# Performance work log

Measured on AMD Instinct MI355X. Metric: run time of the kernel, lower is better.

## Reference

```python
import jax, jax.numpy as jnp
import numpy as np

N = 50000
E = 800000
C = 128          # in = hidden = out channels
R = 16           # num_relations
NB = 4           # num_bases
EPS = 1e-5


def setup_inputs() -> dict:
    key = jax.random.key(0)
    ks = jax.random.split(key, 20)
    node_features = jax.random.normal(ks[0], (N, C), dtype=jnp.float32)
    src = jax.random.randint(ks[1], (E,), 0, N, dtype=jnp.int32)
    rel = jax.random.randint(ks[2], (E,), 0, R, dtype=jnp.int32)
    dst = jax.random.randint(ks[3], (E,), 0, N, dtype=jnp.int32)
    edge_triples = jnp.stack([src, rel, dst], axis=1)  # [E,3]
    s = 0.05
    inp = {
        "node_features": node_features,
        "edge_triples": edge_triples,
        "num_nodes": N,
        "input_w": jax.random.normal(ks[4], (C, C), jnp.float32) * s,
        "input_b": jnp.zeros((C,), jnp.float32),
    }
    for i in range(2):
        k = jax.random.split(ks[5 + i], 4)
        inp[f"basis{i}"] = jax.random.normal(k[0], (NB, C, C), jnp.float32) * s
        inp[f"att{i}"] = jax.random.normal(k[1], (R, NB), jnp.float32) * s
        inp[f"root_w{i}"] = jax.random.normal(k[2], (C, C), jnp.float32) * s
        inp[f"root_b{i}"] = jnp.zeros((C,), jnp.float32)
        inp[f"ln_g{i}"] = jnp.ones((C,), jnp.float32)
        inp[f"ln_b{i}"] = jnp.zeros((C,), jnp.float32)
    return inp


def _layer_norm(x, g, b):
    mu = jnp.mean(x, axis=-1, keepdims=True)
    var = jnp.mean(jnp.square(x - mu), axis=-1, keepdims=True)
    return (x - mu) * jax.lax.rsqrt(var + EPS) * g + b


def _rel_conv(x, edge_triples, num_nodes, basis, att, root_w, root_b):
    # x: [N,C]; basis: [NB,C,O]; att: [R,NB]
    src = edge_triples[:, 0]
    rel = edge_triples[:, 1]
    dst = edge_triples[:, 2]
    # weights = einsum('rb,bio->rio'); messages_e = x[src] @ weights[rel]
    # = sum_b att[rel,b] * (x @ basis[b])[src]  (same math, no [E,C,O] tensor)
    xb = jnp.einsum('ni,bio->bno', x, basis)      # [NB,N,O]
    coef = att[rel]                                # [E,NB]
    out_dim = basis.shape[-1]
    msg = jnp.zeros((src.shape[0], out_dim), x.dtype)
    for b in range(basis.shape[0]):                # small fixed loop over bases
        msg = msg + coef[:, b, None] * xb[b][src]
    deg = jax.ops.segment_sum(jnp.ones_like(dst, dtype=x.dtype), dst,
                              num_segments=num_nodes)
    deg_inv = jnp.where(deg > 0, 1.0 / deg, 0.0)
    msg = msg * deg_inv[dst][:, None]
    out = jax.ops.segment_sum(msg, dst, num_segments=num_nodes)
    return out + x @ root_w + root_b


def reference(node_features, edge_triples, num_nodes, input_w, input_b,
              basis0, att0, root_w0, root_b0, ln_g0, ln_b0,
              basis1, att1, root_w1, root_b1, ln_g1, ln_b1):
    x = node_features @ input_w + input_b
    x = _rel_conv(x, edge_triples, num_nodes, basis0, att0, root_w0, root_b0)
    x = _layer_norm(x, ln_g0, ln_b0)
    x = jax.nn.relu(x)  # dropout is identity in eval mode
    x = _rel_conv(x, edge_triples, num_nodes, basis1, att1, root_w1, root_b1)
    x = _layer_norm(x, ln_g1, ln_b1)
    return x
```

## Files before the change

kernel.cpp:

```cpp
#include <hip/hip_runtime.h>
#include <hip/hip_bf16.h>

#define NN 50000
#define EE 800000

typedef __bf16 bf16x8 __attribute__((ext_vector_type(8)));
typedef float f32x4 __attribute__((ext_vector_type(4)));

__device__ inline float bf2f(unsigned int u) {
    union { unsigned int i; float f; } x; x.i = (u & 0xFFFFu) << 16; return x.f;
}
__device__ inline float bf2fh(unsigned int u) {
    union { unsigned int i; float f; } x; x.i = u & 0xFFFF0000u; return x.f;
}
__device__ inline void bf8_to_f(bf16x8 v, float* f) {
    const unsigned int* u = (const unsigned int*)&v;
    f[0] = bf2f(u[0]); f[1] = bf2fh(u[0]);
    f[2] = bf2f(u[1]); f[3] = bf2fh(u[1]);
    f[4] = bf2f(u[2]); f[5] = bf2fh(u[2]);
    f[6] = bf2f(u[3]); f[7] = bf2fh(u[3]);
}

__global__ void k_zero(int* __restrict__ deg, int* __restrict__ curs) {
    int i = blockIdx.x * 256 + threadIdx.x;
    if (i < NN) { deg[i] = 0; curs[i] = 0; }
}

__global__ void k_deg(const int* __restrict__ et, int* __restrict__ deg) {
    int e = blockIdx.x * 256 + threadIdx.x;
    if (e < EE) atomicAdd(&deg[et[e * 3 + 2]], 1);
}

__global__ void k_scan1(const int* __restrict__ deg, int* __restrict__ incl, int* __restrict__ bsum) {
    __shared__ int s[1024];
    int i = blockIdx.x * 1024 + threadIdx.x;
    int v = (i < NN) ? deg[i] : 0;
    s[threadIdx.x] = v;
    __syncthreads();
    for (int off = 1; off < 1024; off <<= 1) {
        int t = (threadIdx.x >= off) ? s[threadIdx.x - off] : 0;
        __syncthreads();
        s[threadIdx.x] += t;
        __syncthreads();
    }
    if (i < NN) incl[i] = s[threadIdx.x];
    if (threadIdx.x == 1023) bsum[blockIdx.x] = s[1023];
}

__global__ void k_scan2(const int* __restrict__ bsum, int* __restrict__ boff) {
    if (threadIdx.x == 0 && blockIdx.x == 0) {
        int acc = 0;
        for (int i = 0; i < 49; ++i) { boff[i] = acc; acc += bsum[i]; }
    }
}

__global__ void k_scan3(const int* __restrict__ incl, const int* __restrict__ deg,
                        const int* __restrict__ boff, int* __restrict__ row_start) {
    int i = blockIdx.x * 1024 + threadIdx.x;
    if (i < NN) row_start[i] = incl[i] - deg[i] + boff[blockIdx.x];
}

__global__ void k_fill(const int* __restrict__ et, const int* __restrict__ row_start,
                       int* __restrict__ cursor, int* __restrict__ perm) {
    int e = blockIdx.x * 256 + threadIdx.x;
    if (e >= EE) return;
    int src = et[e * 3 + 0];
    int rel = et[e * 3 + 1];
    int dst = et[e * 3 + 2];
    int pos = row_start[dst] + atomicAdd(&cursor[dst], 1);
    perm[pos] = src | (rel << 16);
}

__global__ void k_prep(const float* __restrict__ iw,
                       const float* __restrict__ basis0, const float* __restrict__ rootw0,
                       const float* __restrict__ basis1, const float* __restrict__ rootw1,
                       __bf16* __restrict__ WtInF, __bf16* __restrict__ WtF0, __bf16* __restrict__ WtF1) {
    int t = blockIdx.x * 256 + threadIdx.x;
    if (t < 2048) {
        int lane = t & 63, grp = t >> 6;
        int kk = grp & 3, nblk = grp >> 2;
        int col = nblk * 16 + (lane & 15);
        int k0 = kk * 32 + (lane >> 4) * 8;
        bf16x8 v;
        #pragma unroll
        for (int j = 0; j < 8; ++j) v[j] = (__bf16)iw[(size_t)(k0 + j) * 128 + col];
        *(bf16x8*)(WtInF + (size_t)t * 8) = v;
        return;
    }
    t -= 2048;
    const float* basis = basis0; const float* rootw = rootw0; __bf16* W = WtF0;
    if (t >= 10240) { t -= 10240; basis = basis1; rootw = rootw1; W = WtF1; }
    if (t >= 10240) return;
    int lane = t & 63, grp = t >> 6;
    int kk = grp % 20, nblk = grp / 20;
    int col = nblk * 16 + (lane & 15);
    int k0 = kk * 32 + (lane >> 4) * 8;
    bf16x8 v;
    #pragma unroll
    for (int j = 0; j < 8; ++j) {
        int k = k0 + j;
        float f = (k < 512) ? basis[(size_t)(k >> 7) * 16384 + (size_t)(k & 127) * 128 + col]
                            : rootw[(size_t)(k - 512) * 128 + col];
        v[j] = (__bf16)f;
    }
    *(bf16x8*)(W + (size_t)t * 8) = v;
}

__global__ void k_gemm_in(const float* __restrict__ A, const __bf16* __restrict__ WtInF,
                          const float* __restrict__ bias, __bf16* __restrict__ out, int M) {
    const int tid = threadIdx.x, wave = tid >> 6, lane = tid & 63;
    const int wr = wave >> 1, wc = wave & 1;
    const int l15 = lane & 15, lhi = lane >> 4;
    f32x4 acc[2][4] = {};
    #define LDAI(dst, KK) do { \
        _Pragma("unroll") \
        for (int m = 0; m < 2; ++m) { \
            int rw = blockIdx.x * 64 + wr * 32 + m * 16 + l15; \
            rw = rw < M ? rw : M - 1; \
            const float* ap = A + (size_t)rw * 128 + (KK) * 32 + lhi * 8; \
            float4 v0 = *(const float4*)ap, v1 = *(const float4*)(ap + 4); \
            bf16x8 f; \
            f[0]=(__bf16)v0.x; f[1]=(__bf16)v0.y; f[2]=(__bf16)v0.z; f[3]=(__bf16)v0.w; \
            f[4]=(__bf16)v1.x; f[5]=(__bf16)v1.y; f[6]=(__bf16)v1.z; f[7]=(__bf16)v1.w; \
            dst[m] = f; \
        } } while (0)
    #define LDBI(dst, KK) do { \
        _Pragma("unroll") \
        for (int n = 0; n < 4; ++n) \
            dst[n] = *(const bf16x8*)(WtInF + (((size_t)(wc * 4 + n) * 4 + (KK)) * 64 + lane) * 8); \
        } while (0)
    #define MMI(AA, BB) do { \
        _Pragma("unroll") for (int m = 0; m < 2; ++m) \
        _Pragma("unroll") for (int n = 0; n < 4; ++n) \
            acc[m][n] = __builtin_amdgcn_mfma_f32_16x16x32_bf16(AA[m], BB[n], acc[m][n], 0, 0, 0); \
        } while (0)
    bf16x8 aP[2], bP[4], aQ[2], bQ[4];
    LDAI(aP, 0); LDBI(bP, 0);
    #pragma unroll
    for (int tstep = 0; tstep < 2; ++tstep) {
        LDAI(aQ, 2 * tstep + 1); LDBI(bQ, 2 * tstep + 1);
        MMI(aP, bP);
        if (tstep < 1) { LDAI(aP, 2 * tstep + 2); LDBI(bP, 2 * tstep + 2); }
        MMI(aQ, bQ);
    }
    #pragma unroll
    for (int m = 0; m < 2; ++m)
        #pragma unroll
        for (int j = 0; j < 4; ++j) {
            int row = blockIdx.x * 64 + wr * 32 + m * 16 + lhi * 4 + j;
            if (row >= M) continue;
            #pragma unroll
            for (int n = 0; n < 4; ++n) {
                int col = wc * 64 + n * 16 + l15;
                out[(size_t)row * 128 + col] = (__bf16)(acc[m][n][j] + bias[col]);
            }
        }
}

__global__ void k_agg4(const __bf16* __restrict__ x, const int* __restrict__ perm,
                       const int* __restrict__ rowst, const int* __restrict__ deg,
                       const float* __restrict__ att, __bf16* __restrict__ aggF,
                       int nodeOff, int nodeCnt) {
    __shared__ float4 satt[16];
    if (threadIdx.x < 16) satt[threadIdx.x] = ((const float4*)att)[threadIdx.x];
    __syncthreads();
    int local = blockIdx.x * 4 + (threadIdx.x >> 6);
    if (local >= nodeCnt) return;
    int lane = threadIdx.x & 63;
    int e4 = lane >> 4, c8 = lane & 15;
    int node = nodeOff + local;
    int start = rowst[node], cnt = deg[node];
    float acc[4][8] = {};
    int nIt = (cnt + 3) >> 2;
    for (int it = 0; it < nIt; it += 2) {
        int eA = it * 4 + e4, eB = eA + 4;
        bool vA = eA < cnt, vB = eB < cnt;
        int pA = vA ? perm[start + eA] : 0;
        int pB = vB ? perm[start + eB] : 0;
        bf16x8 uA = *(const bf16x8*)(x + (size_t)(pA & 0xFFFF) * 128 + c8 * 8);
        bf16x8 uB = *(const bf16x8*)(x + (size_t)(pB & 0xFFFF) * 128 + c8 * 8);
        float4 cA = satt[pA >> 16];
        float4 cB = satt[pB >> 16];
        if (!vA) cA = make_float4(0.f, 0.f, 0.f, 0.f);
        if (!vB) cB = make_float4(0.f, 0.f, 0.f, 0.f);
        float fA[8], fB[8];
        bf8_to_f(uA, fA);
        bf8_to_f(uB, fB);
        #pragma unroll
        for (int j = 0; j < 8; ++j) {
            acc[0][j] += cA.x * fA[j]; acc[1][j] += cA.y * fA[j];
            acc[2][j] += cA.z * fA[j]; acc[3][j] += cA.w * fA[j];
        }
        #pragma unroll
        for (int j = 0; j < 8; ++j) {
            acc[0][j] += cB.x * fB[j]; acc[1][j] += cB.y * fB[j];
            acc[2][j] += cB.z * fB[j]; acc[3][j] += cB.w * fB[j];
        }
    }
    float dinv = (cnt > 0) ? 1.f / (float)cnt : 0.f;
    #pragma unroll
    for (int b = 0; b < 4; ++b)
        #pragma unroll
        for (int j = 0; j < 8; ++j) {
            float v = acc[b][j];
            v += __shfl_xor(v, 16);
            v += __shfl_xor(v, 32);
            acc[b][j] = v * dinv;
        }
    bf16x8 o;
    #pragma unroll
    for (int j = 0; j < 8; ++j) {
        float v = (e4 == 0) ? acc[0][j] : (e4 == 1) ? acc[1][j] : (e4 == 2) ? acc[2][j] : acc[3][j];
        o[j] = (__bf16)v;
    }
    size_t idx8 = (((size_t)(local >> 4) * 16 + e4 * 4 + (c8 >> 2)) * 64 + (c8 & 3) * 16 + (local & 15)) * 8;
    *(bf16x8*)(aggF + idx8) = o;
}

template<int OUTF>
__global__ void k_gemm_layer(const __bf16* __restrict__ aggF, const __bf16* __restrict__ x,
                             const __bf16* __restrict__ WtF, const float* __restrict__ rb,
                             const float* __restrict__ g, const float* __restrict__ bb,
                             __bf16* __restrict__ outB, float* __restrict__ outF,
                             int rowOff, int nodeCnt) {
    __shared__ float red[2][2][64];
    __shared__ float murs[2][64];
    const int tid = threadIdx.x, wave = tid >> 6, lane = tid & 63;
    const int wr = wave >> 1, wc = wave & 1;
    const int l15 = lane & 15, lhi = lane >> 4;
    const int rowgrpBase = blockIdx.x * 4 + wr * 2;
    f32x4 acc[2][4] = {};
    #define LDA(dst, KK) do { \
        _Pragma("unroll") \
        for (int m = 0; m < 2; ++m) { \
            if ((KK) < 16) { \
                dst[m] = *(const bf16x8*)(aggF + (((size_t)(rowgrpBase + m) * 16 + (KK)) * 64 + lane) * 8); \
            } else { \
                int rw = blockIdx.x * 64 + wr * 32 + m * 16 + l15; \
                rw = rw < nodeCnt ? rw : nodeCnt - 1; \
                dst[m] = *(const bf16x8*)(x + (size_t)(rowOff + rw) * 128 + ((KK) - 16) * 32 + lhi * 8); \
            } \
        } } while (0)
    #define LDB(dst, KK) do { \
        _Pragma("unroll") \
        for (int n = 0; n < 4; ++n) \
            dst[n] = *(const bf16x8*)(WtF + (((size_t)(wc * 4 + n) * 20 + (KK)) * 64 + lane) * 8); \
        } while (0)
    #define MM(AA, BB) do { \
        _Pragma("unroll") for (int m = 0; m < 2; ++m) \
        _Pragma("unroll") for (int n = 0; n < 4; ++n) \
            acc[m][n] = __builtin_amdgcn_mfma_f32_16x16x32_bf16(AA[m], BB[n], acc[m][n], 0, 0, 0); \
        } while (0)
    bf16x8 aP[2], bP[4], aQ[2], bQ[4];
    LDA(aP, 0); LDB(bP, 0);
    #pragma unroll
    for (int t = 0; t < 10; ++t) {
        LDA(aQ, 2 * t + 1); LDB(bQ, 2 * t + 1);
        MM(aP, bP);
        if (t < 9) { LDA(aP, 2 * t + 2); LDB(bP, 2 * t + 2); }
        MM(aQ, bQ);
    }
    float colb[4];
    #pragma unroll
    for (int n = 0; n < 4; ++n) colb[n] = rb[wc * 64 + n * 16 + l15];
    #pragma unroll
    for (int m = 0; m < 2; ++m)
        #pragma unroll
        for (int j = 0; j < 4; ++j) {
            float s = 0.f, q = 0.f;
            #pragma unroll
            for (int n = 0; n < 4; ++n) {
                float v = acc[m][n][j] + colb[n];
                acc[m][n][j] = v;
                s += v; q += v * v;
            }
            #pragma unroll
            for (int o = 1; o < 16; o <<= 1) { s += __shfl_xor(s, o); q += __shfl_xor(q, o); }
            if (l15 == 0) {
                int r = wr * 32 + m * 16 + lhi * 4 + j;
                red[0][wc][r] = s; red[1][wc][r] = q;
            }
        }
    __syncthreads();
    if (tid < 64) {
        float s = red[0][0][tid] + red[0][1][tid];
        float q = red[1][0][tid] + red[1][1][tid];
        float mu = s * (1.f / 128.f);
        float var = q * (1.f / 128.f) - mu * mu;
        murs[0][tid] = mu;
        murs[1][tid] = rsqrtf(var + 1e-5f);
    }
    __syncthreads();
    float gg[4], gb[4];
    #pragma unroll
    for (int n = 0; n < 4; ++n) {
        int col = wc * 64 + n * 16 + l15;
        gg[n] = g[col]; gb[n] = bb[col];
    }
    #pragma unroll
    for (int m = 0; m < 2; ++m)
        #pragma unroll
        for (int j = 0; j < 4; ++j) {
            int rblk = wr * 32 + m * 16 + lhi * 4 + j;
            int lr = blockIdx.x * 64 + rblk;
            if (lr >= nodeCnt) continue;
            float mu = murs[0][rblk], rs = murs[1][rblk];
            size_t rowbase = (size_t)(rowOff + lr) * 128;
            #pragma unroll
            for (int n = 0; n < 4; ++n) {
                int col = wc * 64 + n * 16 + l15;
                float v = (acc[m][n][j] - mu) * rs * gg[n] + gb[n];
                if (OUTF == 0) { v = fmaxf(v, 0.f); outB[rowbase + col] = (__bf16)v; }
                else           { outF[rowbase + col] = v; }
            }
        }
}

extern "C" void kernel_launch(void* const* d_in, const int* in_sizes, int n_in,
                              void* d_out, int out_size, void* d_ws, size_t ws_size,
                              hipStream_t stream) {
    const float* nf      = (const float*)d_in[0];
    const int*   et      = (const int*)d_in[1];
    const float* input_w = (const float*)d_in[3];
    const float* input_b = (const float*)d_in[4];
    const float* basis0  = (const float*)d_in[5];
    const float* att0    = (const float*)d_in[6];
    const float* rootw0  = (const float*)d_in[7];
    const float* rootb0  = (const float*)d_in[8];
    const float* lng0    = (const float*)d_in[9];
    const float* lnb0    = (const float*)d_in[10];
    const float* basis1  = (const float*)d_in[11];
    const float* att1    = (const float*)d_in[12];
    const float* rootw1  = (const float*)d_in[13];
    const float* rootb1  = (const float*)d_in[14];
    const float* lng1    = (const float*)d_in[15];
    const float* lnb1    = (const float*)d_in[16];
    (void)in_sizes; (void)n_in; (void)out_size;

    char* ws = (char*)d_ws;
    size_t off = 0;
    auto carve = [&](size_t bytes) { char* p = ws + off; off = (off + bytes + 255) & ~(size_t)255; return p; };
    __bf16* x0    = (__bf16*)carve((size_t)NN * 128 * 2);
    __bf16* x1    = (__bf16*)carve((size_t)NN * 128 * 2);
    __bf16* WtInF = (__bf16*)carve((size_t)128 * 128 * 2);
    __bf16* WtF0  = (__bf16*)carve((size_t)128 * 640 * 2);
    __bf16* WtF1  = (__bf16*)carve((size_t)128 * 640 * 2);
    int*    deg   = (int*)carve((size_t)NN * 4);
    int*    incl  = (int*)carve((size_t)NN * 4);
    int*    rowst = (int*)carve((size_t)NN * 4);
    int*    curs  = (int*)carve((size_t)NN * 4);
    int*    bsum  = (int*)carve(64 * 4);
    int*    boff  = (int*)carve(64 * 4);
    int*    perm  = (int*)carve((size_t)EE * 4 + 64);
    size_t remain = (ws_size > off + 4096) ? (ws_size - off - 4096) : 0;
    long long maxNodes = (long long)(remain / 1024);
    int chunkN = (maxNodes >= NN) ? NN : (int)maxNodes;
    if (chunkN < 512) chunkN = 512;
    chunkN = (chunkN + 63) & ~63;
    __bf16* aggF = (__bf16*)carve((size_t)chunkN * 512 * 2);
    int nch = (NN + chunkN - 1) / chunkN;

    k_zero<<<(NN + 255) / 256, 256, 0, stream>>>(deg, curs);
    k_deg<<<(EE + 255) / 256, 256, 0, stream>>>(et, deg);
    k_scan1<<<49, 1024, 0, stream>>>(deg, incl, bsum);
    k_scan2<<<1, 64, 0, stream>>>(bsum, boff);
    k_scan3<<<49, 1024, 0, stream>>>(incl, deg, boff, rowst);
    k_fill<<<(EE + 255) / 256, 256, 0, stream>>>(et, rowst, curs, perm);

    k_prep<<<88, 256, 0, stream>>>(input_w, basis0, rootw0, basis1, rootw1, WtInF, WtF0, WtF1);
    k_gemm_in<<<(NN + 63) / 64, 256, 0, stream>>>(nf, WtInF, input_b, x0, NN);

    for (int c = 0; c < nch; ++c) {
        int o0 = c * chunkN;
        int cnt = (o0 + chunkN <= NN) ? chunkN : (NN - o0);
        k_agg4<<<(cnt + 3) / 4, 256, 0, stream>>>(x0, perm, rowst, deg, att0, aggF, o0, cnt);
        k_gemm_layer<0><<<(cnt + 63) / 64, 256, 0, stream>>>(aggF, x0, WtF0, rootb0, lng0, lnb0,
                                                             x1, nullptr, o0, cnt);
    }

    for (int c = 0; c < nch; ++c) {
        int o0 = c * chunkN;
        int cnt = (o0 + chunkN <= NN) ? chunkN : (NN - o0);
        k_agg4<<<(cnt + 3) / 4, 256, 0, stream>>>(x1, perm, rowst, deg, att1, aggF, o0, cnt);
        k_gemm_layer<1><<<(cnt + 63) / 64, 256, 0, stream>>>(aggF, x1, WtF1, rootb1, lng1, lnb1,
                                                             nullptr, (float*)d_out, o0, cnt);
    }
}
```

Measured before the change: 263.3 us.

## Sort nodes by descending degree and software-pipeline edge gathers in aggregation

Adds a counting sort of nodes by in-degree (histogram, bin scan, scatter), so aggregation processes high-degree nodes first and each block's waves get similar edge counts. The aggregation kernel also double-buffers its gathers, issuing the next 8 edges' feature loads before accumulating the current ones, to hide memory latency. The GEMM/layernorm kernel reads root-term rows and writes output rows through the permutation, which makes those accesses scattered rather than contiguous. It also adds three small kernel launches to the preprocessing.

```diff
diff --git a/kernel.cpp b/kernel.cpp
--- a/kernel.cpp
+++ b/kernel.cpp
@@ -21,9 +21,10 @@
     f[6] = bf2f(u[3]); f[7] = bf2fh(u[3]);
 }
 
-__global__ void k_zero(int* __restrict__ deg, int* __restrict__ curs) {
+__global__ void k_zero(int* __restrict__ deg, int* __restrict__ curs, int* __restrict__ bins) {
     int i = blockIdx.x * 256 + threadIdx.x;
     if (i < NN) { deg[i] = 0; curs[i] = 0; }
+    if (i < 128) bins[i] = 0;
 }
 
 __global__ void k_deg(const int* __restrict__ et, int* __restrict__ deg) {
@@ -69,6 +70,30 @@
     int dst = et[e * 3 + 2];
     int pos = row_start[dst] + atomicAdd(&cursor[dst], 1);
     perm[pos] = src | (rel << 16);
+}
+
+__global__ void k_hist(const int* __restrict__ deg, int* __restrict__ bins) {
+    int i = blockIdx.x * 256 + threadIdx.x;
+    if (i < NN) {
+        int d = deg[i]; d = d > 63 ? 63 : d;
+        atomicAdd(&bins[63 - d], 1);
+    }
+}
+__global__ void k_binscan(const int* __restrict__ bins, int* __restrict__ binoff) {
+    if (threadIdx.x == 0 && blockIdx.x == 0) {
+        int acc = 0;
+        for (int i = 0; i < 64; ++i) { binoff[i] = acc; acc += bins[i]; }
+    }
+}
+__global__ void k_scatter(const int* __restrict__ deg, const int* __restrict__ binoff,
+                          int* __restrict__ bincur, int* __restrict__ order) {
+    int i = blockIdx.x * 256 + threadIdx.x;
+    if (i < NN) {
+        int d = deg[i]; d = d > 63 ? 63 : d;
+        int key = 63 - d;
+        int pos = binoff[key] + atomicAdd(&bincur[key], 1);
+        order[pos] = i;
+    }
 }
 
 __global__ void k_prep(const float* __restrict__ iw,
@@ -157,10 +182,10 @@
         }
 }
 
-__global__ void k_agg4(const __bf16* __restrict__ x, const int* __restrict__ perm,
+__global__ void k_agg5(const __bf16* __restrict__ x, const int* __restrict__ perm,
                        const int* __restrict__ rowst, const int* __restrict__ deg,
-                       const float* __restrict__ att, __bf16* __restrict__ aggF,
-                       int nodeOff, int nodeCnt) {
+                       const float* __restrict__ att, const int* __restrict__ order,
+                       __bf16* __restrict__ aggF, int nodeOff, int nodeCnt) {
     __shared__ float4 satt[16];
     if (threadIdx.x < 16) satt[threadIdx.x] = ((const float4*)att)[threadIdx.x];
     __syncthreads();
@@ -168,33 +193,50 @@
     if (local >= nodeCnt) return;
     int lane = threadIdx.x & 63;
     int e4 = lane >> 4, c8 = lane & 15;
-    int node = nodeOff + local;
+    int node = order[nodeOff + local];
     int start = rowst[node], cnt = deg[node];
     float acc[4][8] = {};
-    int nIt = (cnt + 3) >> 2;
-    for (int it = 0; it < nIt; it += 2) {
-        int eA = it * 4 + e4, eB = eA + 4;
-        bool vA = eA < cnt, vB = eB < cnt;
-        int pA = vA ? perm[start + eA] : 0;
-        int pB = vB ? perm[start + eB] : 0;
-        bf16x8 uA = *(const bf16x8*)(x + (size_t)(pA & 0xFFFF) * 128 + c8 * 8);
-        bf16x8 uB = *(const bf16x8*)(x + (size_t)(pB & 0xFFFF) * 128 + c8 * 8);
-        float4 cA = satt[pA >> 16];
-        float4 cB = satt[pB >> 16];
-        if (!vA) cA = make_float4(0.f, 0.f, 0.f, 0.f);
-        if (!vB) cB = make_float4(0.f, 0.f, 0.f, 0.f);
-        float fA[8], fB[8];
-        bf8_to_f(uA, fA);
-        bf8_to_f(uB, fB);
-        #pragma unroll
-        for (int j = 0; j < 8; ++j) {
-            acc[0][j] += cA.x * fA[j]; acc[1][j] += cA.y * fA[j];
-            acc[2][j] += cA.z * fA[j]; acc[3][j] += cA.w * fA[j];
-        }
-        #pragma unroll
-        for (int j = 0; j < 8; ++j) {
-            acc[0][j] += cB.x * fB[j]; acc[1][j] += cB.y * fB[j];
-            acc[2][j] += cB.z * fB[j]; acc[3][j] += cB.w * fB[j];
+    int nIt = (cnt + 7) >> 3;
+    if (nIt > 0) {
+        bf16x8 uA, uB; float4 cA, cB;
+        {
+            int eA = e4, eB = e4 + 4;
+            bool vA = eA < cnt, vB = eB < cnt;
+            int pA = vA ? perm[start + eA] : 0;
+            int pB = vB ? perm[start + eB] : 0;
+            uA = *(const bf16x8*)(x + (size_t)(pA & 0xFFFF) * 128 + c8 * 8);
+            uB = *(const bf16x8*)(x + (size_t)(pB & 0xFFFF) * 128 + c8 * 8);
+            cA = vA ? satt[pA >> 16] : make_float4(0.f, 0.f, 0.f, 0.f);
+            cB = vB ? satt[pB >> 16] : make_float4(0.f, 0.f, 0.f, 0.f);
+        }
+        for (int s = 0; ; ++s) {
+            bf16x8 nA, nB; float4 nCA, nCB;
+            bool more = (s + 1 < nIt);
+            if (more) {
+                int eA = (s + 1) * 8 + e4, eB = eA + 4;
+                bool vA = eA < cnt, vB = eB < cnt;
+                int pA = vA ? perm[start + eA] : 0;
+                int pB = vB ? perm[start + eB] : 0;
+                nA = *(const bf16x8*)(x + (size_t)(pA & 0xFFFF) * 128 + c8 * 8);
+                nB = *(const bf16x8*)(x + (size_t)(pB & 0xFFFF) * 128 + c8 * 8);
+                nCA = vA ? satt[pA >> 16] : make_float4(0.f, 0.f, 0.f, 0.f);
+                nCB = vB ? satt[pB >> 16] : make_float4(0.f, 0.f, 0.f, 0.f);
+            }
+            float fA[8], fB[8];
+            bf8_to_f(uA, fA);
+            bf8_to_f(uB, fB);
+            #pragma unroll
+            for (int j = 0; j < 8; ++j) {
+                acc[0][j] += cA.x * fA[j]; acc[1][j] += cA.y * fA[j];
+                acc[2][j] += cA.z * fA[j]; acc[3][j] += cA.w * fA[j];
+            }
+            #pragma unroll
+            for (int j = 0; j < 8; ++j) {
+                acc[0][j] += cB.x * fB[j]; acc[1][j] += cB.y * fB[j];
+                acc[2][j] += cB.z * fB[j]; acc[3][j] += cB.w * fB[j];
+            }
+            if (!more) break;
+            uA = nA; uB = nB; cA = nCA; cB = nCB;
         }
     }
     float dinv = (cnt > 0) ? 1.f / (float)cnt : 0.f;
@@ -221,6 +263,7 @@
 __global__ void k_gemm_layer(const __bf16* __restrict__ aggF, const __bf16* __restrict__ x,
                              const __bf16* __restrict__ WtF, const float* __restrict__ rb,
                              const float* __restrict__ g, const float* __restrict__ bb,
+                             const int* __restrict__ order,
                              __bf16* __restrict__ outB, float* __restrict__ outF,
                              int rowOff, int nodeCnt) {
     __shared__ float red[2][2][64];
@@ -229,6 +272,13 @@
     const int wr = wave >> 1, wc = wave & 1;
     const int l15 = lane & 15, lhi = lane >> 4;
     const int rowgrpBase = blockIdx.x * 4 + wr * 2;
+    int ordm[2];
+    #pragma unroll
+    for (int m = 0; m < 2; ++m) {
+        int rw = blockIdx.x * 64 + wr * 32 + m * 16 + l15;
+        rw = rw < nodeCnt ? rw : nodeCnt - 1;
+        ordm[m] = order[rowOff + rw];
+    }
     f32x4 acc[2][4] = {};
     #define LDA(dst, KK) do { \
         _Pragma("unroll") \
@@ -236,9 +286,7 @@
             if ((KK) < 16) { \
                 dst[m] = *(const bf16x8*)(aggF + (((size_t)(rowgrpBase + m) * 16 + (KK)) * 64 + lane) * 8); \
             } else { \
-                int rw = blockIdx.x * 64 + wr * 32 + m * 16 + l15; \
-                rw = rw < nodeCnt ? rw : nodeCnt - 1; \
-                dst[m] = *(const bf16x8*)(x + (size_t)(rowOff + rw) * 128 + ((KK) - 16) * 32 + lhi * 8); \
+                dst[m] = *(const bf16x8*)(x + (size_t)ordm[m] * 128 + ((KK) - 16) * 32 + lhi * 8); \
             } \
         } } while (0)
     #define LDB(dst, KK) do { \
@@ -305,7 +353,8 @@
             int lr = blockIdx.x * 64 + rblk;
             if (lr >= nodeCnt) continue;
             float mu = murs[0][rblk], rs = murs[1][rblk];
-            size_t rowbase = (size_t)(rowOff + lr) * 128;
+            int ord = order[rowOff + lr];
+            size_t rowbase = (size_t)ord * 128;
             #pragma unroll
             for (int n = 0; n < 4; ++n) {
                 int col = wc * 64 + n * 16 + l15;
@@ -349,8 +398,11 @@
     int*    incl  = (int*)carve((size_t)NN * 4);
     int*    rowst = (int*)carve((size_t)NN * 4);
     int*    curs  = (int*)carve((size_t)NN * 4);
+    int*    order = (int*)carve((size_t)NN * 4);
     int*    bsum  = (int*)carve(64 * 4);
     int*    boff  = (int*)carve(64 * 4);
+    int*    bins  = (int*)carve(128 * 4);
+    int*    binoff= (int*)carve(64 * 4);
     int*    perm  = (int*)carve((size_t)EE * 4 + 64);
     size_t remain = (ws_size > off + 4096) ? (ws_size - off - 4096) : 0;
     long long maxNodes = (long long)(remain / 1024);
@@ -360,12 +412,15 @@
     __bf16* aggF = (__bf16*)carve((size_t)chunkN * 512 * 2);
     int nch = (NN + chunkN - 1) / chunkN;
 
-    k_zero<<<(NN + 255) / 256, 256, 0, stream>>>(deg, curs);
+    k_zero<<<(NN + 255) / 256, 256, 0, stream>>>(deg, curs, bins);
     k_deg<<<(EE + 255) / 256, 256, 0, stream>>>(et, deg);
     k_scan1<<<49, 1024, 0, stream>>>(deg, incl, bsum);
     k_scan2<<<1, 64, 0, stream>>>(bsum, boff);
     k_scan3<<<49, 1024, 0, stream>>>(incl, deg, boff, rowst);
     k_fill<<<(EE + 255) / 256, 256, 0, stream>>>(et, rowst, curs, perm);
+    k_hist<<<(NN + 255) / 256, 256, 0, stream>>>(deg, bins);
+    k_binscan<<<1, 64, 0, stream>>>(bins, binoff);
+    k_scatter<<<(NN + 255) / 256, 256, 0, stream>>>(deg, binoff, bins + 64, order);
 
     k_prep<<<88, 256, 0, stream>>>(input_w, basis0, rootw0, basis1, rootw1, WtInF, WtF0, WtF1);
     k_gemm_in<<<(NN + 63) / 64, 256, 0, stream>>>(nf, WtInF, input_b, x0, NN);
@@ -373,16 +428,16 @@
     for (int c = 0; c < nch; ++c) {
         int o0 = c * chunkN;
         int cnt = (o0 + chunkN <= NN) ? chunkN : (NN - o0);
-        k_agg4<<<(cnt + 3) / 4, 256, 0, stream>>>(x0, perm, rowst, deg, att0, aggF, o0, cnt);
+        k_agg5<<<(cnt + 3) / 4, 256, 0, stream>>>(x0, perm, rowst, deg, att0, order, aggF, o0, cnt);
         k_gemm_layer<0><<<(cnt + 63) / 64, 256, 0, stream>>>(aggF, x0, WtF0, rootb0, lng0, lnb0,
-                                                             x1, nullptr, o0, cnt);
+                                                             order, x1, nullptr, o0, cnt);
     }
 
     for (int c = 0; c < nch; ++c) {
         int o0 = c * chunkN;
         int cnt = (o0 + chunkN <= NN) ? chunkN : (NN - o0);
-        k_agg4<<<(cnt + 3) / 4, 256, 0, stream>>>(x1, perm, rowst, deg, att1, aggF, o0, cnt);
+        k_agg5<<<(cnt + 3) / 4, 256, 0, stream>>>(x1, perm, rowst, deg, att1, order, aggF, o0, cnt);
         k_gemm_layer<1><<<(cnt + 63) / 64, 256, 0, stream>>>(aggF, x1, WtF1, rootb1, lng1, lnb1,
-                                                             nullptr, (float*)d_out, o0, cnt);
-    }
-}
+                                                             order, nullptr, (float*)d_out, o0, cnt);
+    }
+}
```

Measured after the change: 558.0 us. +111.9%, slower.
